# Optimization experiments

Hardware: AMD Instinct MI355X
Metric: run time of the kernel (lower is better)

Reference implementation:

```python
import jax, jax.numpy as jnp
import numpy as np

# --- static Cayley table for Cl(3) (8 blades) ---
def _derive_cayley_table():
    basis_gens = [(), (1,), (2,), (3,), (1, 2), (1, 3), (2, 3), (1, 2, 3)]
    gens_to_idx = {g: i for i, g in enumerate(basis_gens)}
    def reduce(a, b):
        gens = list(a) + list(b)
        sign = 1
        changed = True
        while changed:
            changed = False
            i = 0
            while i < len(gens) - 1:
                if gens[i] == gens[i + 1]:
                    gens.pop(i); gens.pop(i)
                    changed = True
                    if i > 0:
                        i -= 1
                elif gens[i] > gens[i + 1]:
                    gens[i], gens[i + 1] = gens[i + 1], gens[i]
                    sign *= -1
                    changed = True
                    i += 1
                else:
                    i += 1
        return gens_to_idx[tuple(gens)], sign
    return [[reduce(basis_gens[i], basis_gens[j]) for j in range(8)] for i in range(8)]

_TAB = _derive_cayley_table()
SI = np.array([i for i in range(8) for _ in range(8)], dtype=np.int32)
SJ = np.array([j for _ in range(8) for j in range(8)], dtype=np.int32)
TK = np.array([_TAB[i][j][0] for i in range(8) for j in range(8)], dtype=np.int32)
SG = np.array([float(_TAB[i][j][1]) for i in range(8) for j in range(8)], dtype=np.float32)

N_TOK, N_BLADE, D_BLADE, D_FFN = 8192, 8, 256, 1024
LN_EPS = 1e-5


def setup_inputs() -> dict:
    key = jax.random.key(0)
    ks = jax.random.split(key, 5)
    scale = 0.02
    return {
        'x': jax.random.normal(ks[0], (N_TOK, N_BLADE, D_BLADE), jnp.float32),
        'interaction_weights': jnp.full((64,), 0.1, jnp.float32),
        'geo_gate': jnp.asarray(0.5, jnp.float32),
        'ln_w': jnp.ones((D_BLADE,), jnp.float32),
        'ln_b': jnp.zeros((D_BLADE,), jnp.float32),
        'W_gate': jax.random.normal(ks[1], (D_BLADE, D_FFN), jnp.float32) * scale,
        'W_up': jax.random.normal(ks[2], (D_BLADE, D_FFN), jnp.float32) * scale,
        'W_down': jax.random.normal(ks[3], (D_FFN, D_BLADE), jnp.float32) * scale,
    }


def reference(x, interaction_weights, geo_gate, ln_w, ln_b, W_gate, W_up, W_down):
    si = jnp.asarray(SI); sj = jnp.asarray(SJ); tk = jnp.asarray(TK)
    sg = jnp.asarray(SG).astype(x.dtype)
    w = jax.nn.sigmoid(interaction_weights).astype(x.dtype)
    # gather blade pairs, weighted Cayley product: (N, 64, D)
    products = x[:, si, :] * x[:, sj, :] * (sg * w)[None, :, None]
    # scatter-add into target blades: (N, 8, D)
    geo = jnp.zeros_like(x).at[:, tk, :].add(products)
    g = jax.nn.sigmoid(geo_gate)
    mixed = g * geo + (1.0 - g) * x
    # LayerNorm over D
    flat = mixed.reshape(-1, x.shape[-1])
    mu = jnp.mean(flat, axis=-1, keepdims=True)
    var = jnp.var(flat, axis=-1, keepdims=True)
    flat = (flat - mu) * jax.lax.rsqrt(var + LN_EPS) * ln_w + ln_b
    # SwiGLU FFN
    h = jax.nn.silu(flat @ W_gate) * (flat @ W_up)
    out = (h @ W_down).reshape(x.shape)
    return x + out
```

## Files before the change

### kernel.cpp

```cpp
#include <hip/hip_runtime.h>
#include <hip/hip_bf16.h>
#include <hip/hip_fp8.h>

typedef __bf16 bf16x8 __attribute__((ext_vector_type(8)));
typedef float floatx4 __attribute__((ext_vector_type(4)));
typedef float floatx16 __attribute__((ext_vector_type(16)));

constexpr int TK[64] = {
  0,1,2,3,4,5,6,7,
  1,0,4,5,2,3,7,6,
  2,4,0,6,1,7,3,5,
  3,5,6,0,7,1,2,4,
  4,2,1,7,0,6,5,3,
  5,3,7,1,6,0,4,2,
  6,7,3,2,5,4,0,1,
  7,6,5,4,3,2,1,0
};
constexpr float SGN[64] = {
  1, 1, 1, 1, 1, 1, 1, 1,
  1, 1, 1, 1, 1, 1, 1, 1,
  1,-1, 1, 1,-1,-1, 1,-1,
  1,-1,-1, 1, 1,-1,-1, 1,
  1,-1, 1, 1,-1,-1, 1,-1,
  1,-1,-1, 1, 1,-1,-1, 1,
  1, 1,-1, 1,-1, 1,-1,-1,
  1, 1,-1, 1,-1, 1,-1,-1
};

__device__ __forceinline__ void async16(const void* g, void* l) {
  __builtin_amdgcn_global_load_lds(
      (const __attribute__((address_space(1))) void*)g,
      (__attribute__((address_space(3))) void*)l, 16, 0, 0);
}

__device__ __forceinline__ unsigned char to_fp8(float v) {
  __hip_fp8_e4m3 q(v);
  return (unsigned char)q.__x;
}

__global__ __launch_bounds__(256) void transpose_cast(
    const float* __restrict__ src, __bf16* __restrict__ dst, int K, int N)
{
  __shared__ float s[32 * 33];
  const int t = threadIdx.x;
  const int k0 = blockIdx.y * 32, n0 = blockIdx.x * 32;
  const int r = t >> 5, c = t & 31;
  #pragma unroll
  for (int i = 0; i < 4; ++i)
    s[(r + i * 8) * 33 + c] = src[(size_t)(k0 + r + i * 8) * N + n0 + c];
  __syncthreads();
  #pragma unroll
  for (int i = 0; i < 4; ++i)
    dst[(size_t)(n0 + r + i * 8) * K + k0 + c] = (__bf16)s[c * 33 + r + i * 8];
}

__global__ __launch_bounds__(256) void transpose_cast_fp8(
    const float* __restrict__ src, unsigned char* __restrict__ dst, int K, int N)
{
  __shared__ float s[32 * 33];
  const int t = threadIdx.x;
  const int k0 = blockIdx.y * 32, n0 = blockIdx.x * 32;
  const int r = t >> 5, c = t & 31;
  #pragma unroll
  for (int i = 0; i < 4; ++i)
    s[(r + i * 8) * 33 + c] = src[(size_t)(k0 + r + i * 8) * N + n0 + c];
  __syncthreads();
  #pragma unroll
  for (int i = 0; i < 4; ++i)
    dst[(size_t)(n0 + r + i * 8) * K + k0 + c] = to_fp8(16.f * s[c * 33 + r + i * 8]);
}

__global__ __launch_bounds__(256) void geo_ln(
    const float* __restrict__ X,
    const float* __restrict__ IW,
    const float* __restrict__ GG,
    const float* __restrict__ LW, const float* __restrict__ LB,
    __bf16* __restrict__ F)
{
  __shared__ float sw[64];
  __shared__ float smix[8 * 256];
  __shared__ float sstat[16];
  const int t = threadIdx.x;
  const int tok = blockIdx.x;

  if (t < 64) sw[t] = SGN[t] / (1.f + __expf(-IW[t]));

  float xv[8];
  #pragma unroll
  for (int b = 0; b < 8; ++b) xv[b] = X[(size_t)tok * 2048 + b * 256 + t];
  const float g = 1.f / (1.f + __expf(-GG[0]));

  __syncthreads();

  float geo[8] = {0.f, 0.f, 0.f, 0.f, 0.f, 0.f, 0.f, 0.f};
  #pragma unroll
  for (int p = 0; p < 64; ++p)
    geo[TK[p]] += xv[p >> 3] * xv[p & 7] * sw[p];

  float mv[8];
  #pragma unroll
  for (int b = 0; b < 8; ++b) {
    mv[b] = g * geo[b] + (1.f - g) * xv[b];
    smix[b * 256 + t] = mv[b];
  }
  __syncthreads();

  const int wv = t >> 6, lane = t & 63;
  #pragma unroll
  for (int s = 0; s < 2; ++s) {
    int b = wv * 2 + s;
    float v0 = smix[b * 256 + lane];
    float v1 = smix[b * 256 + 64 + lane];
    float v2 = smix[b * 256 + 128 + lane];
    float v3 = smix[b * 256 + 192 + lane];
    float sum = v0 + v1 + v2 + v3;
    float sq  = v0*v0 + v1*v1 + v2*v2 + v3*v3;
    #pragma unroll
    for (int off = 32; off > 0; off >>= 1) {
      sum += __shfl_xor(sum, off, 64);
      sq  += __shfl_xor(sq,  off, 64);
    }
    if (lane == 0) {
      float mu  = sum * (1.f / 256.f);
      float var = sq * (1.f / 256.f) - mu * mu;
      sstat[b]     = mu;
      sstat[8 + b] = rsqrtf(var + 1e-5f);
    }
  }
  __syncthreads();

  const float lw = LW[t], lb = LB[t];
  #pragma unroll
  for (int b = 0; b < 8; ++b) {
    float v = (mv[b] - sstat[b]) * sstat[8 + b] * lw + lb;
    F[(size_t)(tok * 8 + b) * 256 + t] = (__bf16)v;
  }
}

__global__ __launch_bounds__(256, 3) void gemm_gateup(
    const __bf16* __restrict__ A,
    const __bf16* __restrict__ Bg,
    const __bf16* __restrict__ Bu,
    unsigned char* __restrict__ H)
{
  __shared__ __align__(16) char smem[32768];
  __bf16* sA  = (__bf16*)smem;
  __bf16* sBg = (__bf16*)(smem + 16384);
  __bf16* sBu = (__bf16*)(smem + 24576);
  int* sD = (int*)(smem + 16384);

  const int t = threadIdx.x;
  const int bid = blockIdx.y * 16 + blockIdx.x;
  const int lid = (bid & 7) * 1024 + (bid >> 3);
  const int f0 = (lid & 15) * 64;
  const int m0 = (lid >> 4) * 128;
  const int lane = t & 63, wv = t >> 6;
  const int wm = wv & 1, wf = wv >> 1;
  const int l31 = lane & 31, half = lane >> 5;

  int aoff[4], boff[2];
  #pragma unroll
  for (int i = 0; i < 4; ++i) {
    int idx = i * 256 + t, row = idx >> 3, slot = idx & 7;
    aoff[i] = (m0 + row) * 256 + (slot ^ (row & 7) ^ ((row >> 3) & 3)) * 8;
  }
  #pragma unroll
  for (int i = 0; i < 2; ++i) {
    int idx = i * 256 + t, row = idx >> 3, slot = idx & 7;
    boff[i] = (f0 + row) * 256 + (slot ^ (row & 7) ^ ((row >> 3) & 3)) * 8;
  }

  floatx16 accg[2], accu[2];
  #pragma unroll
  for (int i = 0; i < 2; ++i)
    #pragma unroll
    for (int r = 0; r < 16; ++r) { accg[i][r] = 0.f; accu[i][r] = 0.f; }

  const int xr = (l31 & 7) ^ ((l31 >> 3) & 3);
  const int rowA0 = (wm * 64 + l31) * 64;
  const int rowA1 = rowA0 + 32 * 64;
  const int rowB  = (wf * 32 + l31) * 64;

  for (int k = 0; k < 4; ++k) {
    const int kk = k * 64;
    #pragma unroll
    for (int i = 0; i < 4; ++i) async16(A + aoff[i] + kk, &sA[(i * 256 + t) * 8]);
    #pragma unroll
    for (int i = 0; i < 2; ++i) {
      async16(Bg + boff[i] + kk, &sBg[(i * 256 + t) * 8]);
      async16(Bu + boff[i] + kk, &sBu[(i * 256 + t) * 8]);
    }
    __syncthreads();

    #pragma unroll
    for (int s = 0; s < 4; ++s) {
      const int oct = ((s * 2 + half) ^ xr) * 8;
      bf16x8 a0 = *(const bf16x8*)&sA[rowA0 + oct];
      bf16x8 a1 = *(const bf16x8*)&sA[rowA1 + oct];
      bf16x8 bg = *(const bf16x8*)&sBg[rowB + oct];
      bf16x8 bu = *(const bf16x8*)&sBu[rowB + oct];
      accg[0] = __builtin_amdgcn_mfma_f32_32x32x16_bf16(bg, a0, accg[0], 0, 0, 0);
      accu[0] = __builtin_amdgcn_mfma_f32_32x32x16_bf16(bu, a0, accu[0], 0, 0, 0);
      accg[1] = __builtin_amdgcn_mfma_f32_32x32x16_bf16(bg, a1, accg[1], 0, 0, 0);
      accu[1] = __builtin_amdgcn_mfma_f32_32x32x16_bf16(bu, a1, accu[1], 0, 0, 0);
    }
    __syncthreads();
  }

  #pragma unroll
  for (int i = 0; i < 2; ++i) {
    const int m_l = wm * 64 + i * 32 + l31;
    #pragma unroll
    for (int q = 0; q < 4; ++q) {
      float hv[4];
      #pragma unroll
      for (int e = 0; e < 4; ++e) {
        float gv = accg[i][q * 4 + e], uv = accu[i][q * 4 + e];
        hv[e] = 16.f * (gv / (1.f + __expf(-gv))) * uv;
      }
      int w = __builtin_amdgcn_cvt_pk_fp8_f32(hv[0], hv[1], 0, false);
      w = __builtin_amdgcn_cvt_pk_fp8_f32(hv[2], hv[3], w, true);
      sD[m_l * 17 + wf * 8 + half + 2 * q] = w;
    }
  }
  __syncthreads();
  #pragma unroll
  for (int c = 0; c < 2; ++c) {
    int chunk = c * 256 + t;
    int m = chunk >> 2, q4 = chunk & 3;
    int4 v;
    v.x = sD[m * 17 + q4 * 4 + 0];
    v.y = sD[m * 17 + q4 * 4 + 1];
    v.z = sD[m * 17 + q4 * 4 + 2];
    v.w = sD[m * 17 + q4 * 4 + 3];
    *(int4*)&H[(size_t)(m0 + m) * 1024 + f0 + q4 * 16] = v;
  }
}

__global__ __launch_bounds__(256, 2) void gemm_down(
    const unsigned char* __restrict__ A,
    const unsigned char* __restrict__ B,
    const float* __restrict__ X,
    float* __restrict__ O)
{
  __shared__ unsigned char sA[128 * 64];
  __shared__ unsigned char sB[256 * 64];
  const int t = threadIdx.x;
  const int m0 = blockIdx.x * 128;
  const int lane = t & 63, wv = t >> 6;
  const int wm = wv & 1, wn = wv >> 1;
  const int l15 = lane & 15, quad = lane >> 4;

  int aoff[2], boff[4];
  #pragma unroll
  for (int i = 0; i < 2; ++i) {
    int idx = i * 256 + t, row = idx >> 2, q = idx & 3;
    aoff[i] = (m0 + row) * 1024 + (q ^ ((row >> 1) & 3)) * 16;
  }
  #pragma unroll
  for (int i = 0; i < 4; ++i) {
    int idx = i * 256 + t, row = idx >> 2, q = idx & 3;
    boff[i] = row * 1024 + (q ^ ((row >> 1) & 3)) * 16;
  }

  floatx4 zero = {0.f, 0.f, 0.f, 0.f};
  floatx4 acc[4][8];
  #pragma unroll
  for (int i = 0; i < 4; ++i)
    #pragma unroll
    for (int j = 0; j < 8; ++j) acc[i][j] = zero;

  int aaddr[2][4], baddr[2][8];
  #pragma unroll
  for (int s = 0; s < 2; ++s) {
    const int u = s * 4 + quad;
    #pragma unroll
    for (int i = 0; i < 4; ++i) {
      int r = wm * 64 + i * 16 + l15;
      aaddr[s][i] = r * 64 + (((u >> 1) ^ ((r >> 1) & 3)) << 4) + (u & 1) * 8;
    }
    #pragma unroll
    for (int j = 0; j < 8; ++j) {
      int r = wn * 128 + j * 16 + l15;
      baddr[s][j] = r * 64 + (((u >> 1) ^ ((r >> 1) & 3)) << 4) + (u & 1) * 8;
    }
  }

  for (int k = 0; k < 16; ++k) {
    const int kk = k * 64;
    #pragma unroll
    for (int i = 0; i < 2; ++i) async16(A + aoff[i] + kk, &sA[(i * 256 + t) * 16]);
    #pragma unroll
    for (int i = 0; i < 4; ++i) async16(B + boff[i] + kk, &sB[(i * 256 + t) * 16]);
    __syncthreads();

    #pragma unroll
    for (int s = 0; s < 2; ++s) {
      long av[4], bv[8];
      #pragma unroll
      for (int i = 0; i < 4; ++i) av[i] = *(const long*)&sA[aaddr[s][i]];
      #pragma unroll
      for (int j = 0; j < 8; ++j) bv[j] = *(const long*)&sB[baddr[s][j]];
      #pragma unroll
      for (int i = 0; i < 4; ++i)
        #pragma unroll
        for (int j = 0; j < 8; ++j)
          acc[i][j] = __builtin_amdgcn_mfma_f32_16x16x32_fp8_fp8(av[i], bv[j], acc[i][j], 0, 0, 0);
    }
    __syncthreads();
  }

  #pragma unroll
  for (int i = 0; i < 4; ++i)
    #pragma unroll
    for (int j = 0; j < 8; ++j)
      #pragma unroll
      for (int r = 0; r < 4; ++r) {
        int m = m0 + wm * 64 + i * 16 + quad * 4 + r;
        int n = wn * 128 + j * 16 + l15;
        size_t o = (size_t)m * 256 + n;
        O[o] = X[o] + acc[i][j][r] * (1.f / 256.f);
      }
}

extern "C" void kernel_launch(void* const* d_in, const int* in_sizes, int n_in,
                              void* d_out, int out_size, void* d_ws, size_t ws_size,
                              hipStream_t stream) {
  const float* x   = (const float*)d_in[0];
  const float* iw  = (const float*)d_in[1];
  const float* gg  = (const float*)d_in[2];
  const float* lnw = (const float*)d_in[3];
  const float* lnb = (const float*)d_in[4];
  const float* Wg  = (const float*)d_in[5];
  const float* Wu  = (const float*)d_in[6];
  const float* Wd  = (const float*)d_in[7];
  float* out = (float*)d_out;

  char* ws = (char*)d_ws;
  __bf16*        flat = (__bf16*)(ws);
  unsigned char* h    = (unsigned char*)(ws + 33554432);
  __bf16*        Bg   = (__bf16*)(ws + 100663296);
  __bf16*        Bu   = (__bf16*)(ws + 101187584);
  unsigned char* Bd   = (unsigned char*)(ws + 101711872);

  transpose_cast<<<dim3(32, 8),  256, 0, stream>>>(Wg, Bg, 256, 1024);
  transpose_cast<<<dim3(32, 8),  256, 0, stream>>>(Wu, Bu, 256, 1024);
  transpose_cast_fp8<<<dim3(8, 32), 256, 0, stream>>>(Wd, Bd, 1024, 256);
  geo_ln<<<8192, 256, 0, stream>>>(x, iw, gg, lnw, lnb, flat);
  gemm_gateup<<<dim3(16, 512), 256, 0, stream>>>(flat, Bg, Bu, h);
  gemm_down<<<512, 256, 0, stream>>>(h, Bd, x, out);
}
```

Before: 279.1 us.

## Merge weight transposes, warp-per-token LayerNorm, double-buffered split-N down GEMM

The three weight transpose/cast kernels become one launch. geo_ln now assigns one wavefront per token with float4 loads and a shuffle-only LayerNorm, which drops the shared-memory round trip and two block barriers. gemm_down is split across two N tiles of 128 to double the block count, uses smaller accumulators for higher occupancy, and double-buffers the LDS async loads so the next k-slice is fetched during the MFMAs. The cost is that each block of gemm_down reloads the H tile for its N half.

```diff
diff --git a/kernel.cpp b/kernel.cpp
--- a/kernel.cpp
+++ b/kernel.cpp
@@ -38,36 +38,38 @@
   return (unsigned char)q.__x;
 }
 
-__global__ __launch_bounds__(256) void transpose_cast(
-    const float* __restrict__ src, __bf16* __restrict__ dst, int K, int N)
+__global__ __launch_bounds__(256) void transpose_all(
+    const float* __restrict__ Wg, const float* __restrict__ Wu,
+    const float* __restrict__ Wd,
+    __bf16* __restrict__ Bg, __bf16* __restrict__ Bu,
+    unsigned char* __restrict__ Bd)
 {
   __shared__ float s[32 * 33];
+  const int z = blockIdx.y;
+  const int b = blockIdx.x;
   const int t = threadIdx.x;
-  const int k0 = blockIdx.y * 32, n0 = blockIdx.x * 32;
   const int r = t >> 5, c = t & 31;
-  #pragma unroll
-  for (int i = 0; i < 4; ++i)
-    s[(r + i * 8) * 33 + c] = src[(size_t)(k0 + r + i * 8) * N + n0 + c];
-  __syncthreads();
-  #pragma unroll
-  for (int i = 0; i < 4; ++i)
-    dst[(size_t)(n0 + r + i * 8) * K + k0 + c] = (__bf16)s[c * 33 + r + i * 8];
-}
-
-__global__ __launch_bounds__(256) void transpose_cast_fp8(
-    const float* __restrict__ src, unsigned char* __restrict__ dst, int K, int N)
-{
-  __shared__ float s[32 * 33];
-  const int t = threadIdx.x;
-  const int k0 = blockIdx.y * 32, n0 = blockIdx.x * 32;
-  const int r = t >> 5, c = t & 31;
-  #pragma unroll
-  for (int i = 0; i < 4; ++i)
-    s[(r + i * 8) * 33 + c] = src[(size_t)(k0 + r + i * 8) * N + n0 + c];
-  __syncthreads();
-  #pragma unroll
-  for (int i = 0; i < 4; ++i)
-    dst[(size_t)(n0 + r + i * 8) * K + k0 + c] = to_fp8(16.f * s[c * 33 + r + i * 8]);
+  if (z < 2) {
+    const float* src = z ? Wu : Wg;
+    __bf16* dst = z ? Bu : Bg;
+    const int n0 = (b & 31) * 32, k0 = (b >> 5) * 32;
+    #pragma unroll
+    for (int i = 0; i < 4; ++i)
+      s[(r + i * 8) * 33 + c] = src[(size_t)(k0 + r + i * 8) * 1024 + n0 + c];
+    __syncthreads();
+    #pragma unroll
+    for (int i = 0; i < 4; ++i)
+      dst[(size_t)(n0 + r + i * 8) * 256 + k0 + c] = (__bf16)s[c * 33 + r + i * 8];
+  } else {
+    const int n0 = (b & 7) * 32, k0 = (b >> 3) * 32;
+    #pragma unroll
+    for (int i = 0; i < 4; ++i)
+      s[(r + i * 8) * 33 + c] = Wd[(size_t)(k0 + r + i * 8) * 256 + n0 + c];
+    __syncthreads();
+    #pragma unroll
+    for (int i = 0; i < 4; ++i)
+      Bd[(size_t)(n0 + r + i * 8) * 1024 + k0 + c] = to_fp8(16.f * s[c * 33 + r + i * 8]);
+  }
 }
 
 __global__ __launch_bounds__(256) void geo_ln(
@@ -78,62 +80,46 @@
     __bf16* __restrict__ F)
 {
   __shared__ float sw[64];
-  __shared__ float smix[8 * 256];
-  __shared__ float sstat[16];
   const int t = threadIdx.x;
-  const int tok = blockIdx.x;
+  const int wv = t >> 6, lane = t & 63;
+  const int tok = blockIdx.x * 4 + wv;
 
   if (t < 64) sw[t] = SGN[t] / (1.f + __expf(-IW[t]));
-
-  float xv[8];
-  #pragma unroll
-  for (int b = 0; b < 8; ++b) xv[b] = X[(size_t)tok * 2048 + b * 256 + t];
   const float g = 1.f / (1.f + __expf(-GG[0]));
 
+  floatx4 xv[8];
+  #pragma unroll
+  for (int b = 0; b < 8; ++b)
+    xv[b] = *(const floatx4*)&X[(size_t)tok * 2048 + b * 256 + lane * 4];
+  const floatx4 lw4 = *(const floatx4*)&LW[lane * 4];
+  const floatx4 lb4 = *(const floatx4*)&LB[lane * 4];
+
   __syncthreads();
 
-  float geo[8] = {0.f, 0.f, 0.f, 0.f, 0.f, 0.f, 0.f, 0.f};
+  floatx4 geo[8];
+  #pragma unroll
+  for (int b = 0; b < 8; ++b) geo[b] = floatx4{0.f, 0.f, 0.f, 0.f};
   #pragma unroll
   for (int p = 0; p < 64; ++p)
     geo[TK[p]] += xv[p >> 3] * xv[p & 7] * sw[p];
 
-  float mv[8];
   #pragma unroll
   for (int b = 0; b < 8; ++b) {
-    mv[b] = g * geo[b] + (1.f - g) * xv[b];
-    smix[b * 256 + t] = mv[b];
-  }
-  __syncthreads();
-
-  const int wv = t >> 6, lane = t & 63;
-  #pragma unroll
-  for (int s = 0; s < 2; ++s) {
-    int b = wv * 2 + s;
-    float v0 = smix[b * 256 + lane];
-    float v1 = smix[b * 256 + 64 + lane];
-    float v2 = smix[b * 256 + 128 + lane];
-    float v3 = smix[b * 256 + 192 + lane];
-    float sum = v0 + v1 + v2 + v3;
-    float sq  = v0*v0 + v1*v1 + v2*v2 + v3*v3;
+    floatx4 m4 = g * geo[b] + (1.f - g) * xv[b];
+    float s = m4[0] + m4[1] + m4[2] + m4[3];
+    float q = m4[0]*m4[0] + m4[1]*m4[1] + m4[2]*m4[2] + m4[3]*m4[3];
     #pragma unroll
     for (int off = 32; off > 0; off >>= 1) {
-      sum += __shfl_xor(sum, off, 64);
-      sq  += __shfl_xor(sq,  off, 64);
-    }
-    if (lane == 0) {
-      float mu  = sum * (1.f / 256.f);
-      float var = sq * (1.f / 256.f) - mu * mu;
-      sstat[b]     = mu;
-      sstat[8 + b] = rsqrtf(var + 1e-5f);
-    }
-  }
-  __syncthreads();
-
-  const float lw = LW[t], lb = LB[t];
-  #pragma unroll
-  for (int b = 0; b < 8; ++b) {
-    float v = (mv[b] - sstat[b]) * sstat[8 + b] * lw + lb;
-    F[(size_t)(tok * 8 + b) * 256 + t] = (__bf16)v;
+      s += __shfl_xor(s, off, 64);
+      q += __shfl_xor(q, off, 64);
+    }
+    float mu = s * (1.f / 256.f);
+    float rstd = rsqrtf(q * (1.f / 256.f) - mu * mu + 1e-5f);
+    floatx4 v = (m4 - mu) * rstd * lw4 + lb4;
+    union { __bf16 h[4]; short4 s4; } u;
+    u.h[0] = (__bf16)v[0]; u.h[1] = (__bf16)v[1];
+    u.h[2] = (__bf16)v[2]; u.h[3] = (__bf16)v[3];
+    *(short4*)&F[(size_t)(tok * 8 + b) * 256 + lane * 4] = u.s4;
   }
 }
 
@@ -237,40 +223,37 @@
   }
 }
 
-__global__ __launch_bounds__(256, 2) void gemm_down(
+__global__ __launch_bounds__(256, 4) void gemm_down(
     const unsigned char* __restrict__ A,
     const unsigned char* __restrict__ B,
     const float* __restrict__ X,
     float* __restrict__ O)
 {
-  __shared__ unsigned char sA[128 * 64];
-  __shared__ unsigned char sB[256 * 64];
+  __shared__ unsigned char sH[2][8192];
+  __shared__ unsigned char sW[2][8192];
   const int t = threadIdx.x;
-  const int m0 = blockIdx.x * 128;
+  const int m0 = blockIdx.y * 128;
+  const int n0 = blockIdx.x * 128;
   const int lane = t & 63, wv = t >> 6;
   const int wm = wv & 1, wn = wv >> 1;
   const int l15 = lane & 15, quad = lane >> 4;
 
-  int aoff[2], boff[4];
+  int aoff[2], boff[2];
   #pragma unroll
   for (int i = 0; i < 2; ++i) {
     int idx = i * 256 + t, row = idx >> 2, q = idx & 3;
     aoff[i] = (m0 + row) * 1024 + (q ^ ((row >> 1) & 3)) * 16;
-  }
-  #pragma unroll
-  for (int i = 0; i < 4; ++i) {
-    int idx = i * 256 + t, row = idx >> 2, q = idx & 3;
-    boff[i] = row * 1024 + (q ^ ((row >> 1) & 3)) * 16;
+    boff[i] = (n0 + row) * 1024 + (q ^ ((row >> 1) & 3)) * 16;
   }
 
   floatx4 zero = {0.f, 0.f, 0.f, 0.f};
-  floatx4 acc[4][8];
+  floatx4 acc[4][4];
   #pragma unroll
   for (int i = 0; i < 4; ++i)
     #pragma unroll
-    for (int j = 0; j < 8; ++j) acc[i][j] = zero;
-
-  int aaddr[2][4], baddr[2][8];
+    for (int j = 0; j < 4; ++j) acc[i][j] = zero;
+
+  int aaddr[2][4], baddr[2][4];
   #pragma unroll
   for (int s = 0; s < 2; ++s) {
     const int u = s * 4 + quad;
@@ -280,44 +263,53 @@
       aaddr[s][i] = r * 64 + (((u >> 1) ^ ((r >> 1) & 3)) << 4) + (u & 1) * 8;
     }
     #pragma unroll
-    for (int j = 0; j < 8; ++j) {
-      int r = wn * 128 + j * 16 + l15;
+    for (int j = 0; j < 4; ++j) {
+      int r = wn * 64 + j * 16 + l15;
       baddr[s][j] = r * 64 + (((u >> 1) ^ ((r >> 1) & 3)) << 4) + (u & 1) * 8;
     }
   }
 
+  #pragma unroll
+  for (int i = 0; i < 2; ++i) {
+    async16(A + aoff[i], &sH[0][(i * 256 + t) * 16]);
+    async16(B + boff[i], &sW[0][(i * 256 + t) * 16]);
+  }
+
   for (int k = 0; k < 16; ++k) {
-    const int kk = k * 64;
-    #pragma unroll
-    for (int i = 0; i < 2; ++i) async16(A + aoff[i] + kk, &sA[(i * 256 + t) * 16]);
-    #pragma unroll
-    for (int i = 0; i < 4; ++i) async16(B + boff[i] + kk, &sB[(i * 256 + t) * 16]);
-    __syncthreads();
+    const int cur = k & 1;
+    __syncthreads();
+    if (k < 15) {
+      const int kk = (k + 1) * 64, nb = cur ^ 1;
+      #pragma unroll
+      for (int i = 0; i < 2; ++i) {
+        async16(A + aoff[i] + kk, &sH[nb][(i * 256 + t) * 16]);
+        async16(B + boff[i] + kk, &sW[nb][(i * 256 + t) * 16]);
+      }
+    }
 
     #pragma unroll
     for (int s = 0; s < 2; ++s) {
-      long av[4], bv[8];
-      #pragma unroll
-      for (int i = 0; i < 4; ++i) av[i] = *(const long*)&sA[aaddr[s][i]];
-      #pragma unroll
-      for (int j = 0; j < 8; ++j) bv[j] = *(const long*)&sB[baddr[s][j]];
+      long av[4], bv[4];
+      #pragma unroll
+      for (int i = 0; i < 4; ++i) av[i] = *(const long*)&sH[cur][aaddr[s][i]];
+      #pragma unroll
+      for (int j = 0; j < 4; ++j) bv[j] = *(const long*)&sW[cur][baddr[s][j]];
       #pragma unroll
       for (int i = 0; i < 4; ++i)
         #pragma unroll
-        for (int j = 0; j < 8; ++j)
+        for (int j = 0; j < 4; ++j)
           acc[i][j] = __builtin_amdgcn_mfma_f32_16x16x32_fp8_fp8(av[i], bv[j], acc[i][j], 0, 0, 0);
     }
-    __syncthreads();
   }
 
   #pragma unroll
   for (int i = 0; i < 4; ++i)
     #pragma unroll
-    for (int j = 0; j < 8; ++j)
+    for (int j = 0; j < 4; ++j)
       #pragma unroll
       for (int r = 0; r < 4; ++r) {
         int m = m0 + wm * 64 + i * 16 + quad * 4 + r;
-        int n = wn * 128 + j * 16 + l15;
+        int n = n0 + wn * 64 + j * 16 + l15;
         size_t o = (size_t)m * 256 + n;
         O[o] = X[o] + acc[i][j][r] * (1.f / 256.f);
       }
@@ -343,10 +335,8 @@
   __bf16*        Bu   = (__bf16*)(ws + 101187584);
   unsigned char* Bd   = (unsigned char*)(ws + 101711872);
 
-  transpose_cast<<<dim3(32, 8),  256, 0, stream>>>(Wg, Bg, 256, 1024);
-  transpose_cast<<<dim3(32, 8),  256, 0, stream>>>(Wu, Bu, 256, 1024);
-  transpose_cast_fp8<<<dim3(8, 32), 256, 0, stream>>>(Wd, Bd, 1024, 256);
-  geo_ln<<<8192, 256, 0, stream>>>(x, iw, gg, lnw, lnb, flat);
+  transpose_all<<<dim3(256, 3), 256, 0, stream>>>(Wg, Wu, Wd, Bg, Bu, Bd);
+  geo_ln<<<2048, 256, 0, stream>>>(x, iw, gg, lnw, lnb, flat);
   gemm_gateup<<<dim3(16, 512), 256, 0, stream>>>(flat, Bg, Bu, h);
-  gemm_down<<<512, 256, 0, stream>>>(h, Bd, x, out);
-}
+  gemm_down<<<dim3(2, 512), 256, 0, stream>>>(h, Bd, x, out);
+}
```

Result: no change. 275.7 us (-1.2%).
